# Kernel optimization log

Hardware: AMD Instinct MI355X
Metric: run time of the kernel (lower is better)

## Reference

```python
import jax, jax.numpy as jnp
import numpy as np

K = 8                     # block_size
EPS_MIN, EPS_MAX = 2.0, 15.0
ROUND_M, ROUND_N = 10, 10
TEMP = 50.0               # round_temperature
INIT_QUALITY = 90

STD_LUMA = np.array([[16,11,10,16,24,40,51,61],[12,12,14,19,26,58,60,55],[14,13,16,24,40,57,69,56],[14,17,22,29,51,87,80,62],[18,22,37,56,68,109,103,77],[24,35,55,64,81,104,113,92],[49,64,78,87,103,121,120,101],[72,92,95,98,112,100,103,99]], dtype=np.float32)
STD_CHROMA = np.array([[17,18,24,47,99,99,99,99],[18,21,26,66,99,99,99,99],[24,26,56,99,99,99,99,99],[47,66,99,99,99,99,99,99],[99,99,99,99,99,99,99,99],[99,99,99,99,99,99,99,99],[99,99,99,99,99,99,99,99],[99,99,99,99,99,99,99,99]], dtype=np.float32)

def _quality_to_table(base, quality):
    scale = 5000.0 / quality if quality < 50 else 200.0 - 2.0 * quality
    return np.clip(np.floor((base * scale + 50.0) / 100.0), 1.0, 255.0).astype(np.float32)

def _dct_matrix(k):
    n = np.arange(k)
    mat = np.sqrt(2.0 / k) * np.cos((2 * n[None, :] + 1) * n[:, None] * np.pi / (2.0 * k))
    mat[0, :] = np.sqrt(1.0 / k)
    return jnp.asarray(mat, dtype=jnp.float32)

DCT = _dct_matrix(K)  # (K, K)

def _soft_round(x):
    # Differentiable staircase round over integer range [-M, N]:
    # round(x) ~= -M + sum_{k=-M}^{N-1} sigmoid(T * (x - k - 0.5))
    ks = jnp.arange(-ROUND_M, ROUND_N, dtype=jnp.float32)
    return -float(ROUND_M) + jnp.sum(jax.nn.sigmoid(TEMP * (x[..., None] - ks - 0.5)), axis=-1)

def setup_inputs() -> dict:
    key = jax.random.key(0)
    k_img, _ = jax.random.split(key)
    images = jax.random.uniform(k_img, (8, 3, 512, 512), dtype=jnp.float32)
    q_y = jnp.asarray(_quality_to_table(STD_LUMA, INIT_QUALITY))
    q_c = jnp.asarray(_quality_to_table(STD_CHROMA, INIT_QUALITY))
    return {"images": images, "q_y": q_y, "q_c": q_c}

def reference(images, q_y, q_c):
    x = jnp.clip(images, 0.0, 1.0)
    B, C, H, W = x.shape  # H, W are multiples of K (no padding needed)
    # RGB -> YCbCr
    r, g, b = x[:, 0:1], x[:, 1:2], x[:, 2:3]
    y  =  0.299 * r + 0.587 * g + 0.114 * b
    cb = -0.168736 * r - 0.331264 * g + 0.5 * b + 0.5
    cr =  0.5 * r - 0.418688 * g - 0.081312 * b + 0.5
    yc = jnp.concatenate([y, cb, cr], axis=1)
    # blockwise layout: (B, C, H/K, W/K, K, K)
    blocks = yc.reshape(B, C, H // K, K, W // K, K).transpose(0, 1, 2, 4, 3, 5)
    # 2D DCT per original code convention: coef = D @ X @ D (note: NOT D X D^T)
    coef = jnp.einsum('ij,bcuvjk,kl->bcuvil', DCT, blocks, DCT)
    # clamped learnable quant tables; chroma table shared by Cb and Cr
    qy = jnp.clip(q_y, EPS_MIN, EPS_MAX)
    qc = jnp.clip(q_c, EPS_MIN, EPS_MAX)
    qt = jnp.stack([qy, qc, qc])[None, :, None, None]  # (1,3,1,1,K,K)
    quant = _soft_round(coef / qt) * qt
    # 2D IDCT: rec = D^T @ X @ D^T (inverse of the above convention)
    rec = jnp.einsum('ji,bcuvjk,lk->bcuvil', DCT, quant, DCT)
    rec = rec.transpose(0, 1, 2, 4, 3, 5).reshape(B, C, H, W)
    # YCbCr -> RGB
    y2, cb2, cr2 = rec[:, 0:1], rec[:, 1:2] - 0.5, rec[:, 2:3] - 0.5
    r2 = y2 + 1.402 * cr2
    g2 = y2 - 0.344136 * cb2 - 0.714136 * cr2
    b2 = y2 + 1.772 * cb2
    out = jnp.concatenate([r2, g2, b2], axis=1)
    return jnp.clip(out, 0.0, 1.0)
```

## Files before the change

kernel.cpp:

```cpp
#include <hip/hip_runtime.h>
#include <math.h>

namespace {

constexpr int LDSS = 76;

struct DctMat {
  float d[8][8];
  constexpr DctMat() : d{} {
    const float CT[17] = {
        1.0f, 0.9807852804032304f, 0.9238795325112867f, 0.8314696123025452f,
        0.7071067811865476f, 0.5555702330196022f, 0.3826834323650898f,
        0.19509032201612825f, 0.0f, -0.19509032201612825f,
        -0.3826834323650898f, -0.5555702330196022f, -0.7071067811865476f,
        -0.8314696123025452f, -0.9238795325112867f, -0.9807852804032304f,
        -1.0f};
    for (int i = 0; i < 8; ++i)
      for (int j = 0; j < 8; ++j) {
        if (i == 0) {
          d[i][j] = 0.35355339059327373f;
        } else {
          int m = ((2 * j + 1) * i) % 32;
          if (m > 16) m = 32 - m;
          d[i][j] = 0.5f * CT[m];
        }
      }
  }
};
constexpr DctMat DM{};

template <bool TRANSPOSED>
__device__ __forceinline__ void mul8(const float (&a)[8], float (&t)[8]) {
#pragma unroll
  for (int i = 0; i < 8; ++i) {
    float s = 0.0f;
#pragma unroll
    for (int j = 0; j < 8; ++j) {
      s = fmaf(a[j], TRANSPOSED ? DM.d[j][i] : DM.d[i][j], s);
    }
    t[i] = s;
  }
}

__device__ __forceinline__ void transpose3(float (&T)[3][8], float* lds, int blk,
                                           int r) {
#pragma unroll
  for (int c = 0; c < 3; ++c) {
    float* lp = lds + (c * 8 + blk) * LDSS;
#pragma unroll
    for (int j = 0; j < 8; ++j) lp[j * 8 + r] = T[c][j];
  }
  __syncthreads();
#pragma unroll
  for (int c = 0; c < 3; ++c) {
    const float* lp = lds + (c * 8 + blk) * LDSS + r * 8;
    float4 v0 = *reinterpret_cast<const float4*>(lp);
    float4 v1 = *reinterpret_cast<const float4*>(lp + 4);
    T[c][0] = v0.x; T[c][1] = v0.y; T[c][2] = v0.z; T[c][3] = v0.w;
    T[c][4] = v1.x; T[c][5] = v1.y; T[c][6] = v1.z; T[c][7] = v1.w;
  }
  __syncthreads();
}

__device__ __forceinline__ void quant8(float (&a)[8], const float (&q)[8]) {
#pragma unroll
  for (int i = 0; i < 8; ++i) {
    float qv = q[i];
    float x = a[i] * __builtin_amdgcn_rcpf(qv);
    float kc = floorf(x);
    kc = fmaxf(-10.0f, fminf(9.0f, kc));
    float arg = 50.0f * (x - kc - 0.5f);
    float e = __expf(-arg);
    float sr = kc + __builtin_amdgcn_rcpf(1.0f + e);
    a[i] = sr * qv;
  }
}

__device__ __forceinline__ void load8(const float* __restrict__ p, float (&a)[8]) {
  float4 v0 = *reinterpret_cast<const float4*>(p);
  float4 v1 = *reinterpret_cast<const float4*>(p + 4);
  a[0] = v0.x; a[1] = v0.y; a[2] = v0.z; a[3] = v0.w;
  a[4] = v1.x; a[5] = v1.y; a[6] = v1.z; a[7] = v1.w;
}

__device__ __forceinline__ void store8(float* __restrict__ p, const float (&a)[8]) {
  float4 v0 = {a[0], a[1], a[2], a[3]};
  float4 v1 = {a[4], a[5], a[6], a[7]};
  *reinterpret_cast<float4*>(p) = v0;
  *reinterpret_cast<float4*>(p + 4) = v1;
}

__global__ __launch_bounds__(64) void jpeg_kernel(
    const float* __restrict__ img, const float* __restrict__ qy,
    const float* __restrict__ qc, float* __restrict__ out) {
  __shared__ float lds[3 * 8 * LDSS];

  const int lane = threadIdx.x;
  const int blk = lane & 7;
  const int r = lane >> 3;

  const int w = blockIdx.x;
  const int b = w >> 9;
  const int rr = w & 511;
  const int u = rr >> 3;
  const int v0 = (rr & 7) << 3;

  const int row = u * 8 + r;
  const int col = (v0 + blk) * 8;

  const size_t ims = 512 * 512;
  const float* pbase = img + (size_t)b * 3 * ims + (size_t)row * 512 + col;

  float R[8], G[8], B[8];
  load8(pbase, R);
  load8(pbase + ims, G);
  load8(pbase + 2 * ims, B);

  float qycol[8], qccol[8];
#pragma unroll
  for (int i = 0; i < 8; ++i) {
    qycol[i] = fminf(fmaxf(qy[i * 8 + r], 2.0f), 15.0f);
    qccol[i] = fminf(fmaxf(qc[i * 8 + r], 2.0f), 15.0f);
  }

  float A[3][8];
#pragma unroll
  for (int i = 0; i < 8; ++i) {
    float rv = fminf(fmaxf(R[i], 0.0f), 1.0f);
    float gv = fminf(fmaxf(G[i], 0.0f), 1.0f);
    float bv = fminf(fmaxf(B[i], 0.0f), 1.0f);
    A[0][i] = 0.299f * rv + 0.587f * gv + 0.114f * bv;
    A[1][i] = -0.168736f * rv - 0.331264f * gv + 0.5f * bv + 0.5f;
    A[2][i] = 0.5f * rv - 0.418688f * gv - 0.081312f * bv + 0.5f;
  }

  float T[3][8];
#pragma unroll
  for (int c = 0; c < 3; ++c) mul8<true>(A[c], T[c]);
  transpose3(T, lds, blk, r);
#pragma unroll
  for (int c = 0; c < 3; ++c) mul8<false>(T[c], A[c]);

  quant8(A[0], qycol);
  quant8(A[1], qccol);
  quant8(A[2], qccol);

#pragma unroll
  for (int c = 0; c < 3; ++c) mul8<true>(A[c], T[c]);
  transpose3(T, lds, blk, r);
#pragma unroll
  for (int c = 0; c < 3; ++c) mul8<false>(T[c], A[c]);

  float R2[8], G2[8], B2[8];
#pragma unroll
  for (int i = 0; i < 8; ++i) {
    float y2 = A[0][i];
    float cb2 = A[1][i] - 0.5f;
    float cr2 = A[2][i] - 0.5f;
    float r2 = y2 + 1.402f * cr2;
    float g2 = y2 - 0.344136f * cb2 - 0.714136f * cr2;
    float b2 = y2 + 1.772f * cb2;
    R2[i] = fminf(fmaxf(r2, 0.0f), 1.0f);
    G2[i] = fminf(fmaxf(g2, 0.0f), 1.0f);
    B2[i] = fminf(fmaxf(b2, 0.0f), 1.0f);
  }

  float* obase = out + (size_t)b * 3 * ims + (size_t)row * 512 + col;
  store8(obase, R2);
  store8(obase + ims, G2);
  store8(obase + 2 * ims, B2);
}

}

extern "C" void kernel_launch(void* const* d_in, const int* in_sizes, int n_in,
                              void* d_out, int out_size, void* d_ws, size_t ws_size,
                              hipStream_t stream) {
  const float* img = (const float*)d_in[0];
  const float* qy = (const float*)d_in[1];
  const float* qc = (const float*)d_in[2];
  float* out = (float*)d_out;
  jpeg_kernel<<<dim3(4096), dim3(64), 0, stream>>>(img, qy, qc, out);
}
```

Baseline: 82.17 us.

## Split color channels across three wavefronts with LDS color exchange

Each block now runs 192 threads, one wavefront per color channel. The RGB to YCbCr conversion and its inverse go through LDS, so each wave does the DCT, quantisation and IDCT for only its own channel. The per-wave transpose uses an lgkmcnt wait in place of a block barrier. The quantiser also drops the floor clamp and hoists the reciprocal of the quant table. The goal is to cut per-thread register pressure and raise parallelism, at the cost of extra LDS traffic and block-level syncs. Removing the clamp relies on coefficients staying inside the soft-round range.

Result: no change. 82.29 us (+0.1%).

```diff
diff --git a/kernel.cpp b/kernel.cpp
--- a/kernel.cpp
+++ b/kernel.cpp
@@ -4,6 +4,7 @@
 namespace {
 
 constexpr int LDSS = 76;
+constexpr int CSTR = 8 * LDSS;
 
 struct DctMat {
   float d[8][8];
@@ -42,40 +43,6 @@
   }
 }
 
-__device__ __forceinline__ void transpose3(float (&T)[3][8], float* lds, int blk,
-                                           int r) {
-#pragma unroll
-  for (int c = 0; c < 3; ++c) {
-    float* lp = lds + (c * 8 + blk) * LDSS;
-#pragma unroll
-    for (int j = 0; j < 8; ++j) lp[j * 8 + r] = T[c][j];
-  }
-  __syncthreads();
-#pragma unroll
-  for (int c = 0; c < 3; ++c) {
-    const float* lp = lds + (c * 8 + blk) * LDSS + r * 8;
-    float4 v0 = *reinterpret_cast<const float4*>(lp);
-    float4 v1 = *reinterpret_cast<const float4*>(lp + 4);
-    T[c][0] = v0.x; T[c][1] = v0.y; T[c][2] = v0.z; T[c][3] = v0.w;
-    T[c][4] = v1.x; T[c][5] = v1.y; T[c][6] = v1.z; T[c][7] = v1.w;
-  }
-  __syncthreads();
-}
-
-__device__ __forceinline__ void quant8(float (&a)[8], const float (&q)[8]) {
-#pragma unroll
-  for (int i = 0; i < 8; ++i) {
-    float qv = q[i];
-    float x = a[i] * __builtin_amdgcn_rcpf(qv);
-    float kc = floorf(x);
-    kc = fmaxf(-10.0f, fminf(9.0f, kc));
-    float arg = 50.0f * (x - kc - 0.5f);
-    float e = __expf(-arg);
-    float sr = kc + __builtin_amdgcn_rcpf(1.0f + e);
-    a[i] = sr * qv;
-  }
-}
-
 __device__ __forceinline__ void load8(const float* __restrict__ p, float (&a)[8]) {
   float4 v0 = *reinterpret_cast<const float4*>(p);
   float4 v1 = *reinterpret_cast<const float4*>(p + 4);
@@ -90,12 +57,52 @@
   *reinterpret_cast<float4*>(p + 4) = v1;
 }
 
-__global__ __launch_bounds__(64) void jpeg_kernel(
+__device__ __forceinline__ void load8_lds(const float* p, float (&a)[8]) {
+  float4 v0 = *reinterpret_cast<const float4*>(p);
+  float4 v1 = *reinterpret_cast<const float4*>(p + 4);
+  a[0] = v0.x; a[1] = v0.y; a[2] = v0.z; a[3] = v0.w;
+  a[4] = v1.x; a[5] = v1.y; a[6] = v1.z; a[7] = v1.w;
+}
+
+__device__ __forceinline__ void store8_lds(float* p, const float (&a)[8]) {
+  float4 v0 = {a[0], a[1], a[2], a[3]};
+  float4 v1 = {a[4], a[5], a[6], a[7]};
+  *reinterpret_cast<float4*>(p) = v0;
+  *reinterpret_cast<float4*>(p + 4) = v1;
+}
+
+__device__ __forceinline__ void transpose1(float (&T)[8], float* lp, int r) {
+#pragma unroll
+  for (int j = 0; j < 8; ++j) lp[j * 8 + r] = T[j];
+  asm volatile("s_waitcnt lgkmcnt(0)" ::: "memory");
+  __builtin_amdgcn_sched_barrier(0);
+  const float* rp = lp + r * 8;
+  float4 v0 = *reinterpret_cast<const float4*>(rp);
+  float4 v1 = *reinterpret_cast<const float4*>(rp + 4);
+  T[0] = v0.x; T[1] = v0.y; T[2] = v0.z; T[3] = v0.w;
+  T[4] = v1.x; T[5] = v1.y; T[6] = v1.z; T[7] = v1.w;
+}
+
+__device__ __forceinline__ void quant8(float (&a)[8], const float (&q)[8],
+                                       const float (&rq)[8]) {
+#pragma unroll
+  for (int i = 0; i < 8; ++i) {
+    float x = a[i] * rq[i];
+    float kc = floorf(x);
+    float arg = 50.0f * (x - kc - 0.5f);
+    float e = __expf(-arg);
+    float sr = kc + __builtin_amdgcn_rcpf(1.0f + e);
+    a[i] = sr * q[i];
+  }
+}
+
+__global__ __launch_bounds__(192) void jpeg_kernel(
     const float* __restrict__ img, const float* __restrict__ qy,
     const float* __restrict__ qc, float* __restrict__ out) {
-  __shared__ float lds[3 * 8 * LDSS];
-
-  const int lane = threadIdx.x;
+  __shared__ float lds[3 * CSTR];
+
+  const int c = __builtin_amdgcn_readfirstlane(threadIdx.x >> 6);
+  const int lane = threadIdx.x & 63;
   const int blk = lane & 7;
   const int r = lane >> 3;
 
@@ -109,66 +116,86 @@
   const int col = (v0 + blk) * 8;
 
   const size_t ims = 512 * 512;
-  const float* pbase = img + (size_t)b * 3 * ims + (size_t)row * 512 + col;
-
-  float R[8], G[8], B[8];
-  load8(pbase, R);
-  load8(pbase + ims, G);
-  load8(pbase + 2 * ims, B);
-
-  float qycol[8], qccol[8];
+  const size_t poff = ((size_t)b * 3 + c) * ims + (size_t)row * 512 + col;
+
+  float X[8];
+  load8(img + poff, X);
+
+  const float* qt = (c == 0) ? qy : qc;
+  float qcol[8], rqcol[8];
 #pragma unroll
   for (int i = 0; i < 8; ++i) {
-    qycol[i] = fminf(fmaxf(qy[i * 8 + r], 2.0f), 15.0f);
-    qccol[i] = fminf(fmaxf(qc[i * 8 + r], 2.0f), 15.0f);
-  }
-
-  float A[3][8];
-#pragma unroll
-  for (int i = 0; i < 8; ++i) {
-    float rv = fminf(fmaxf(R[i], 0.0f), 1.0f);
-    float gv = fminf(fmaxf(G[i], 0.0f), 1.0f);
-    float bv = fminf(fmaxf(B[i], 0.0f), 1.0f);
-    A[0][i] = 0.299f * rv + 0.587f * gv + 0.114f * bv;
-    A[1][i] = -0.168736f * rv - 0.331264f * gv + 0.5f * bv + 0.5f;
-    A[2][i] = 0.5f * rv - 0.418688f * gv - 0.081312f * bv + 0.5f;
-  }
-
-  float T[3][8];
-#pragma unroll
-  for (int c = 0; c < 3; ++c) mul8<true>(A[c], T[c]);
-  transpose3(T, lds, blk, r);
-#pragma unroll
-  for (int c = 0; c < 3; ++c) mul8<false>(T[c], A[c]);
-
-  quant8(A[0], qycol);
-  quant8(A[1], qccol);
-  quant8(A[2], qccol);
-
-#pragma unroll
-  for (int c = 0; c < 3; ++c) mul8<true>(A[c], T[c]);
-  transpose3(T, lds, blk, r);
-#pragma unroll
-  for (int c = 0; c < 3; ++c) mul8<false>(T[c], A[c]);
-
-  float R2[8], G2[8], B2[8];
-#pragma unroll
-  for (int i = 0; i < 8; ++i) {
-    float y2 = A[0][i];
-    float cb2 = A[1][i] - 0.5f;
-    float cr2 = A[2][i] - 0.5f;
-    float r2 = y2 + 1.402f * cr2;
-    float g2 = y2 - 0.344136f * cb2 - 0.714136f * cr2;
-    float b2 = y2 + 1.772f * cb2;
-    R2[i] = fminf(fmaxf(r2, 0.0f), 1.0f);
-    G2[i] = fminf(fmaxf(g2, 0.0f), 1.0f);
-    B2[i] = fminf(fmaxf(b2, 0.0f), 1.0f);
-  }
-
-  float* obase = out + (size_t)b * 3 * ims + (size_t)row * 512 + col;
-  store8(obase, R2);
-  store8(obase + ims, G2);
-  store8(obase + 2 * ims, B2);
+    float qv = fminf(fmaxf(qt[i * 8 + r], 2.0f), 15.0f);
+    qcol[i] = qv;
+    rqcol[i] = __builtin_amdgcn_rcpf(qv);
+  }
+
+#pragma unroll
+  for (int i = 0; i < 8; ++i) X[i] = fminf(fmaxf(X[i], 0.0f), 1.0f);
+  float* sp = lds + c * CSTR + r * LDSS + blk * 8;
+  store8_lds(sp, X);
+  __syncthreads();
+
+  float A[8];
+  {
+    float Rv[8], Gv[8], Bv[8];
+    const float* rp0 = lds + r * LDSS + blk * 8;
+    load8_lds(rp0, Rv);
+    load8_lds(rp0 + CSTR, Gv);
+    load8_lds(rp0 + 2 * CSTR, Bv);
+    if (c == 0) {
+#pragma unroll
+      for (int i = 0; i < 8; ++i)
+        A[i] = fmaf(0.299f, Rv[i], fmaf(0.587f, Gv[i], 0.114f * Bv[i]));
+    } else if (c == 1) {
+#pragma unroll
+      for (int i = 0; i < 8; ++i)
+        A[i] = fmaf(-0.168736f, Rv[i], fmaf(-0.331264f, Gv[i], fmaf(0.5f, Bv[i], 0.5f)));
+    } else {
+#pragma unroll
+      for (int i = 0; i < 8; ++i)
+        A[i] = fmaf(0.5f, Rv[i], fmaf(-0.418688f, Gv[i], fmaf(-0.081312f, Bv[i], 0.5f)));
+    }
+  }
+  __syncthreads();
+
+  float T[8];
+  float* tp = lds + (c * 8 + blk) * LDSS;
+  mul8<true>(A, T);
+  transpose1(T, tp, r);
+  mul8<false>(T, A);
+
+  quant8(A, qcol, rqcol);
+
+  mul8<true>(A, T);
+  transpose1(T, tp, r);
+  mul8<false>(T, A);
+
+  store8_lds(sp, A);
+  __syncthreads();
+
+  {
+    float Yv[8], Cbv[8], Crv[8];
+    const float* rp0 = lds + r * LDSS + blk * 8;
+    load8_lds(rp0, Yv);
+    load8_lds(rp0 + CSTR, Cbv);
+    load8_lds(rp0 + 2 * CSTR, Crv);
+    float O[8];
+    if (c == 0) {
+#pragma unroll
+      for (int i = 0; i < 8; ++i) O[i] = fmaf(1.402f, Crv[i], Yv[i] - 0.701f);
+    } else if (c == 1) {
+#pragma unroll
+      for (int i = 0; i < 8; ++i)
+        O[i] = fmaf(-0.344136f, Cbv[i], fmaf(-0.714136f, Crv[i], Yv[i] + 0.529136f));
+    } else {
+#pragma unroll
+      for (int i = 0; i < 8; ++i) O[i] = fmaf(1.772f, Cbv[i], Yv[i] - 0.886f);
+    }
+#pragma unroll
+    for (int i = 0; i < 8; ++i) O[i] = fminf(fmaxf(O[i], 0.0f), 1.0f);
+    store8(out + poff, O);
+  }
 }
 
 }
@@ -180,5 +207,5 @@
   const float* qy = (const float*)d_in[1];
   const float* qc = (const float*)d_in[2];
   float* out = (float*)d_out;
-  jpeg_kernel<<<dim3(4096), dim3(64), 0, stream>>>(img, qy, qc, out);
-}
+  jpeg_kernel<<<dim3(4096), dim3(192), 0, stream>>>(img, qy, qc, out);
+}
```
